# Kernel tuning notes

Measured on AMD Instinct MI355X. Metric: run time of the kernel, lower is better.

## Reference

```python
import jax, jax.numpy as jnp
import numpy as np

D_MODEL = 512
NUM_HEADS = 8
D_K = D_MODEL // NUM_HEADS  # 64
LN_EPS = 1e-5


def setup_inputs() -> dict:
    key = jax.random.key(0)
    ks = jax.random.split(key, 6)
    B, S, D = 8, 1024, D_MODEL
    scale = 1.0 / np.sqrt(D)
    return {
        "query": jax.random.normal(ks[0], (B, S, D), jnp.float32),
        "key": jax.random.normal(ks[1], (B, S, D), jnp.float32),
        "value": jax.random.normal(ks[2], (B, S, D), jnp.float32),
        "Wq": jax.random.normal(ks[3], (D, D), jnp.float32) * scale,
        "bq": jnp.zeros((D,), jnp.float32),
        "Wk": jax.random.normal(ks[4], (D, D), jnp.float32) * scale,
        "bk": jnp.zeros((D,), jnp.float32),
        "Wo": jax.random.normal(ks[5], (D, D * NUM_HEADS), jnp.float32) * (1.0 / np.sqrt(D * NUM_HEADS)),
        "bo": jnp.zeros((D,), jnp.float32),
        "gamma": jnp.ones((D,), jnp.float32),
        "beta": jnp.zeros((D,), jnp.float32),
    }


def reference(query, key, value, Wq, bq, Wk, bk, Wo, bo, gamma, beta):
    B, S, D = value.shape
    h, dk = NUM_HEADS, D_K
    # QK projections -> [B, h, S, dk]
    q = (query @ Wq.T + bq).reshape(B, S, h, dk).transpose(0, 2, 1, 3)
    k = (key @ Wk.T + bk).reshape(B, S, h, dk).transpose(0, 2, 1, 3)
    # scaled dot-product scores [B, h, Sq, Sk]
    scores = jnp.einsum("bhqd,bhkd->bhqk", q, k) / jnp.sqrt(jnp.asarray(dk, q.dtype))
    attn = jax.nn.softmax(scores, axis=-1)
    # value broadcast across heads: value is [B, Sk, D] -> per-head output [B, h, Sq, D]
    x = jnp.einsum("bhqk,bkd->bhqd", attn, value)
    # concat heads -> [B, Sq, h*D], output projection back to D
    x = x.transpose(0, 2, 1, 3).reshape(B, S, h * D)
    x = x @ Wo.T + bo
    # residual + LayerNorm (dropout = identity in eval)
    y = value + x
    mu = jnp.mean(y, axis=-1, keepdims=True)
    var = jnp.var(y, axis=-1, keepdims=True)
    out = (y - mu) * jax.lax.rsqrt(var + LN_EPS) * gamma + beta
    return out, attn
```

## Files before the change

### kernel.cpp

```cpp
#include <hip/hip_runtime.h>
#include <hip/hip_bf16.h>

#define B_ 8
#define S_ 1024
#define D_ 512
#define H_ 8
#define DK_ 64
#define HD_ 4096

typedef __attribute__((ext_vector_type(8))) short bf16x8;
typedef __attribute__((ext_vector_type(4))) float f32x4;

static __device__ __forceinline__ unsigned short f2bf(float f) {
    unsigned u = __float_as_uint(f);
    unsigned r = (u + 0x7fffu + ((u >> 16) & 1u)) >> 16;
    return (unsigned short)r;
}

static __device__ __forceinline__ void gload16(const unsigned short* g, unsigned short* l) {
    __builtin_amdgcn_global_load_lds(
        (const __attribute__((address_space(1))) void*)g,
        (__attribute__((address_space(3))) void*)l, 16, 0, 0);
}

static __device__ __forceinline__ int plidx(int ql, int k) {
    return ql * 1024 + ((((k >> 3) ^ (ql & 7))) << 3) + (k & 7);
}

__global__ __launch_bounds__(256) void cvt_kernel(
    const float* __restrict__ src, unsigned short* __restrict__ dst)
{
    const size_t i = ((size_t)blockIdx.x * 256 + threadIdx.x) * 4;
    float4 v = *(const float4*)&src[i];
    ushort4 u = { f2bf(v.x), f2bf(v.y), f2bf(v.z), f2bf(v.w) };
    *(ushort4*)&dst[i] = u;
}

__global__ __launch_bounds__(256) void cvt2_kernel(
    const float* __restrict__ s0, unsigned short* __restrict__ d0,
    const float* __restrict__ s1, unsigned short* __restrict__ d1, int nb0)
{
    const bool first = (int)blockIdx.x < nb0;
    const float* s = first ? s0 : s1;
    unsigned short* d = first ? d0 : d1;
    const int bid = first ? blockIdx.x : blockIdx.x - nb0;
    const size_t i = ((size_t)bid * 256 + threadIdx.x) * 4;
    float4 v = *(const float4*)&s[i];
    ushort4 u = { f2bf(v.x), f2bf(v.y), f2bf(v.z), f2bf(v.w) };
    *(ushort4*)&d[i] = u;
}

__global__ __launch_bounds__(256) void vt_kernel(
    const float* __restrict__ V, unsigned short* __restrict__ Vt)
{
    __shared__ float tile[32][33];
    const int b = blockIdx.z, s0 = blockIdx.x * 32, e0 = blockIdx.y * 32;
    const int t = threadIdx.x;
    const int r = t >> 3, c4 = (t & 7) * 4;
    float4 v = *(const float4*)&V[((size_t)b * S_ + s0 + r) * D_ + e0 + c4];
    tile[r][c4 + 0] = v.x; tile[r][c4 + 1] = v.y;
    tile[r][c4 + 2] = v.z; tile[r][c4 + 3] = v.w;
    __syncthreads();
    ushort4 u;
    u.x = f2bf(tile[c4 + 0][r]); u.y = f2bf(tile[c4 + 1][r]);
    u.z = f2bf(tile[c4 + 2][r]); u.w = f2bf(tile[c4 + 3][r]);
    *(ushort4*)&Vt[((size_t)b * D_ + e0 + r) * S_ + s0 + c4] = u;
}

template<int KDIM, int TN, int MODE>
__global__ __launch_bounds__(256) void gemm_t(
    const unsigned short* __restrict__ A, const unsigned short* __restrict__ Bw,
    const float* __restrict__ bias, const float* __restrict__ Vres,
    void* __restrict__ Out, float scale)
{
    constexpr int NB = 512 / TN;
    constexpr int CF = TN / 32;
    const int o = blockIdx.x;
    const int cpx = gridDim.x / 8;
    const int nb = (o % 8) * cpx + o / 8;
    const int m0 = (nb / NB) * 128;
    const int n0 = (nb % NB) * TN;

    __shared__ __align__(16) unsigned short As[2][128 * 32];
    __shared__ __align__(16) unsigned short Bs[2][TN * 32];

    const int t = threadIdx.x;
    const int wave = t >> 6, lane = t & 63;
    const int wr = wave >> 1, wc = wave & 1;
    const int lr = lane & 15, g = lane >> 4;
    const int gx = (g ^ (lr & 3)) << 3;

    f32x4 acc[4][CF];
    #pragma unroll
    for (int r = 0; r < 4; ++r)
        #pragma unroll
        for (int c = 0; c < CF; ++c) acc[r][c] = (f32x4){0.f, 0.f, 0.f, 0.f};

    const int sub = lane >> 2;
    const int cb  = (((lane & 3) ^ (sub & 3)) << 3);

    auto stage = [&](int buf, int k0) {
        #pragma unroll
        for (int s = 0; s < 2; ++s) {
            const int chunk = s * 4 + wave;
            const int row = chunk * 16 + sub;
            if constexpr (MODE == 0) {
                gload16(&A[(size_t)(m0 + row) * KDIM + k0 + cb], &As[buf][chunk * 512]);
            } else {
                const int m = m0 + row;
                const int bb = m >> 10, ss = m & 1023;
                const int h = k0 >> 9;
                gload16(&A[(((size_t)(bb * H_ + h)) * S_ + ss) * D_ + (k0 & 511) + cb],
                        &As[buf][chunk * 512]);
            }
        }
        #pragma unroll
        for (int s = 0; s < TN / 64; ++s) {
            const int chunk = s * 4 + wave;
            const int row = chunk * 16 + sub;
            gload16(&Bw[(size_t)(n0 + row) * KDIM + k0 + cb], &Bs[buf][chunk * 512]);
        }
    };
    auto compute = [&](int cur) {
        bf16x8 af[4], bfr[CF];
        #pragma unroll
        for (int r = 0; r < 4; ++r)
            af[r] = *(const bf16x8*)&As[cur][(wr * 64 + r * 16 + lr) * 32 + gx];
        #pragma unroll
        for (int c = 0; c < CF; ++c)
            bfr[c] = *(const bf16x8*)&Bs[cur][(wc * (TN / 2) + c * 16 + lr) * 32 + gx];
        __builtin_amdgcn_s_setprio(1);
        #pragma unroll
        for (int c = 0; c < CF; ++c)
            #pragma unroll
            for (int r = 0; r < 4; ++r)
                acc[r][c] = __builtin_amdgcn_mfma_f32_16x16x32_bf16(af[r], bfr[c], acc[r][c], 0, 0, 0);
        __builtin_amdgcn_s_setprio(0);
    };

    const int NT = KDIM / 32;
    stage(0, 0);
    __syncthreads();
    int cur = 0;
    for (int tt = 0; tt < NT - 1; ++tt) {
        stage(cur ^ 1, (tt + 1) * 32);
        compute(cur);
        __syncthreads();
        cur ^= 1;
    }
    compute(cur);

    float bn[CF];
    #pragma unroll
    for (int c = 0; c < CF; ++c) bn[c] = bias[n0 + wc * (TN / 2) + c * 16 + lr];

    #pragma unroll
    for (int r = 0; r < 4; ++r) {
        #pragma unroll
        for (int c = 0; c < CF; ++c) {
            const int n = n0 + wc * (TN / 2) + c * 16 + lr;
            #pragma unroll
            for (int i = 0; i < 4; ++i) {
                const int m = m0 + wr * 64 + r * 16 + g * 4 + i;
                if constexpr (MODE == 0) {
                    const int srow = m & 1023, bb = m >> 10;
                    const int h = n >> 6, dk = n & 63;
                    ((unsigned short*)Out)[(((size_t)(bb * H_ + h)) * S_ + srow) * DK_ + dk] =
                        f2bf((acc[r][c][i] + bn[c]) * scale);
                } else {
                    const size_t oo = (size_t)m * D_ + n;
                    ((float*)Out)[oo] = acc[r][c][i] + bn[c] + Vres[oo];
                }
            }
        }
    }
}

__global__ __launch_bounds__(1024, 4) void fused_attn(
    const unsigned short* __restrict__ Qbf,
    const unsigned short* __restrict__ Kbf,
    const unsigned short* __restrict__ Vt,
    float* __restrict__ attn,
    unsigned short* __restrict__ AV)
{
    const int o = blockIdx.x;
    const int nb = (o & 7) * 128 + (o >> 3);
    const int bh = nb >> 4;
    const int q0 = (nb & 15) * 64;
    const int b = bh >> 3;
    const unsigned short* Qb = Qbf + (size_t)bh * S_ * DK_;
    const unsigned short* Kb = Kbf + (size_t)bh * S_ * DK_;
    const unsigned short* Vb = Vt + (size_t)b * D_ * S_;
    float* outp = attn + ((size_t)bh << 20);

    __shared__ unsigned short PL[64 * 1024];
    __shared__ float redm[64][16];
    __shared__ float rowm[64];

    const int t = threadIdx.x;
    const int wave = t >> 6, lane = t & 63;
    const int wcol = wave * 64;
    const int lr = lane & 15;
    const int g  = lane >> 4;

    f32x4 acc[4][4];
    #pragma unroll
    for (int r = 0; r < 4; ++r)
        #pragma unroll
        for (int c = 0; c < 4; ++c) acc[r][c] = (f32x4){0.f, 0.f, 0.f, 0.f};

    #pragma unroll
    for (int kk = 0; kk < 2; ++kk) {
        bf16x8 af[4];
        #pragma unroll
        for (int r = 0; r < 4; ++r)
            af[r] = *(const bf16x8*)&Kb[(size_t)(wcol + r * 16 + lr) * DK_ + kk * 32 + g * 8];
        bf16x8 qf[4];
        #pragma unroll
        for (int c = 0; c < 4; ++c)
            qf[c] = *(const bf16x8*)&Qb[(size_t)(q0 + c * 16 + lr) * DK_ + kk * 32 + g * 8];
        __builtin_amdgcn_s_setprio(1);
        #pragma unroll
        for (int r = 0; r < 4; ++r)
            #pragma unroll
            for (int c = 0; c < 4; ++c)
                acc[r][c] = __builtin_amdgcn_mfma_f32_16x16x32_bf16(af[r], qf[c], acc[r][c], 0, 0, 0);
        __builtin_amdgcn_s_setprio(0);
    }

    float mloc[4];
    #pragma unroll
    for (int c = 0; c < 4; ++c) {
        float m = acc[0][c][0];
        #pragma unroll
        for (int r = 0; r < 4; ++r)
            #pragma unroll
            for (int i = 0; i < 4; ++i) m = fmaxf(m, acc[r][c][i]);
        m = fmaxf(m, __shfl_xor(m, 16));
        m = fmaxf(m, __shfl_xor(m, 32));
        mloc[c] = m;
    }
    if (lane < 16) {
        #pragma unroll
        for (int c = 0; c < 4; ++c) redm[c * 16 + lane][wave] = mloc[c];
    }
    __syncthreads();
    if (t < 64) {
        float m = redm[t][0];
        #pragma unroll
        for (int w = 1; w < 16; ++w) m = fmaxf(m, redm[t][w]);
        rowm[t] = m;
    }
    __syncthreads();
    float sloc[4];
    #pragma unroll
    for (int c = 0; c < 4; ++c) {
        const float m = rowm[c * 16 + lr];
        float s = 0.f;
        #pragma unroll
        for (int r = 0; r < 4; ++r)
            #pragma unroll
            for (int i = 0; i < 4; ++i) {
                float p = __expf(acc[r][c][i] - m);
                acc[r][c][i] = p;
                s += p;
            }
        s += __shfl_xor(s, 16);
        s += __shfl_xor(s, 32);
        sloc[c] = s;
    }
    __syncthreads();
    if (lane < 16) {
        #pragma unroll
        for (int c = 0; c < 4; ++c) redm[c * 16 + lane][wave] = sloc[c];
    }
    __syncthreads();
    if (t < 64) {
        float s = redm[t][0];
        #pragma unroll
        for (int w = 1; w < 16; ++w) s += redm[t][w];
        rowm[t] = 1.0f / s;
    }
    __syncthreads();

    #pragma unroll
    for (int c = 0; c < 4; ++c) {
        const int ql = c * 16 + lr;
        const float ri = rowm[ql];
        #pragma unroll
        for (int r = 0; r < 4; ++r) {
            f32x4 v = acc[r][c];
            v[0] *= ri; v[1] *= ri; v[2] *= ri; v[3] *= ri;
            const int k = wcol + r * 16 + g * 4;
            unsigned p01, p23;
            asm("v_cvt_pk_bf16_f32 %0, %1, %2" : "=v"(p01) : "v"(v[0]), "v"(v[1]));
            asm("v_cvt_pk_bf16_f32 %0, %1, %2" : "=v"(p23) : "v"(v[2]), "v"(v[3]));
            uint2 pk = { p01, p23 };
            *(uint2*)&PL[plidx(ql, k)] = pk;
        }
    }
    __syncthreads();

    #pragma unroll
    for (int jj = 0; jj < 4; ++jj) {
        const int row = wave * 4 + jj;
        const int ps = lane ^ (row & 7);
        float* rowp = outp + ((size_t)(q0 + row) << 10);
        uint4 u0 = *(const uint4*)&PL[row * 1024 + (ps << 3)];
        uint4 u1 = *(const uint4*)&PL[row * 1024 + ((64 + ps) << 3)];
        f32x4 f0, f1, f2, f3;
        f0[0] = __uint_as_float((u0.x & 0xffffu) << 16);
        f0[1] = __uint_as_float(u0.x & 0xffff0000u);
        f0[2] = __uint_as_float((u0.y & 0xffffu) << 16);
        f0[3] = __uint_as_float(u0.y & 0xffff0000u);
        f1[0] = __uint_as_float((u0.z & 0xffffu) << 16);
        f1[1] = __uint_as_float(u0.z & 0xffff0000u);
        f1[2] = __uint_as_float((u0.w & 0xffffu) << 16);
        f1[3] = __uint_as_float(u0.w & 0xffff0000u);
        f2[0] = __uint_as_float((u1.x & 0xffffu) << 16);
        f2[1] = __uint_as_float(u1.x & 0xffff0000u);
        f2[2] = __uint_as_float((u1.y & 0xffffu) << 16);
        f2[3] = __uint_as_float(u1.y & 0xffff0000u);
        f3[0] = __uint_as_float((u1.z & 0xffffu) << 16);
        f3[1] = __uint_as_float(u1.z & 0xffff0000u);
        f3[2] = __uint_as_float((u1.w & 0xffffu) << 16);
        f3[3] = __uint_as_float(u1.w & 0xffff0000u);
        const int k0f = lane * 8;
        __builtin_nontemporal_store(f0, (f32x4*)&rowp[k0f]);
        __builtin_nontemporal_store(f1, (f32x4*)&rowp[k0f + 4]);
        __builtin_nontemporal_store(f2, (f32x4*)&rowp[512 + k0f]);
        __builtin_nontemporal_store(f3, (f32x4*)&rowp[512 + k0f + 4]);
    }

    const int we = wave * 32;
    f32x4 accv[4][2];
    #pragma unroll
    for (int r = 0; r < 4; ++r)
        #pragma unroll
        for (int c = 0; c < 2; ++c) accv[r][c] = (f32x4){0.f, 0.f, 0.f, 0.f};

    const unsigned short* vp0 = Vb + (size_t)(we + lr) * S_ + g * 8;
    const unsigned short* vp1 = Vb + (size_t)(we + 16 + lr) * S_ + g * 8;
    bf16x8 vf0 = *(const bf16x8*)vp0;
    bf16x8 vf1 = *(const bf16x8*)vp1;

    for (int k0 = 0; k0 < S_; k0 += 32) {
        bf16x8 nv0, nv1;
        const int kn = k0 + 32;
        if (kn < S_) {
            nv0 = *(const bf16x8*)(vp0 + kn);
            nv1 = *(const bf16x8*)(vp1 + kn);
        }
        bf16x8 pa[4];
        #pragma unroll
        for (int r = 0; r < 4; ++r)
            pa[r] = *(const bf16x8*)&PL[plidx(r * 16 + lr, k0 + g * 8)];
        __builtin_amdgcn_s_setprio(1);
        #pragma unroll
        for (int r = 0; r < 4; ++r)
            accv[r][0] = __builtin_amdgcn_mfma_f32_16x16x32_bf16(pa[r], vf0, accv[r][0], 0, 0, 0);
        #pragma unroll
        for (int r = 0; r < 4; ++r)
            accv[r][1] = __builtin_amdgcn_mfma_f32_16x16x32_bf16(pa[r], vf1, accv[r][1], 0, 0, 0);
        __builtin_amdgcn_s_setprio(0);
        if (kn < S_) { vf0 = nv0; vf1 = nv1; }
    }

    __syncthreads();
    unsigned short* PL2 = PL;
    #pragma unroll
    for (int r = 0; r < 4; ++r)
        #pragma unroll
        for (int c = 0; c < 2; ++c) {
            const int e = we + c * 16 + lr;
            #pragma unroll
            for (int i = 0; i < 4; ++i) {
                const int row = r * 16 + g * 4 + i;
                PL2[row * 520 + e] = f2bf(accv[r][c][i]);
            }
        }
    __syncthreads();
    {
        const int row = t >> 4;
        unsigned short* avp = AV + ((size_t)bh * S_ + q0 + row) * D_;
        #pragma unroll
        for (int j = 0; j < 4; ++j) {
            const int e0 = (t & 15) * 8 + j * 128;
            uint4 u = *(const uint4*)&PL2[row * 520 + e0];
            *(uint4*)&avp[e0] = u;
        }
    }
}

__global__ __launch_bounds__(256) void ln_kernel(
    float* __restrict__ Y, const float* __restrict__ gamma,
    const float* __restrict__ beta)
{
    const int lane = threadIdx.x & 63;
    const int wave = threadIdx.x >> 6;
    const size_t row = (size_t)blockIdx.x * 4 + wave;
    float* p = Y + row * D_;
    float4 v0 = *(float4*)&p[lane * 4];
    float4 v1 = *(float4*)&p[256 + lane * 4];
    float s = v0.x + v0.y + v0.z + v0.w + v1.x + v1.y + v1.z + v1.w;
    float q = v0.x * v0.x + v0.y * v0.y + v0.z * v0.z + v0.w * v0.w +
              v1.x * v1.x + v1.y * v1.y + v1.z * v1.z + v1.w * v1.w;
    #pragma unroll
    for (int m = 1; m < 64; m <<= 1) {
        s += __shfl_xor(s, m);
        q += __shfl_xor(q, m);
    }
    const float mu  = s * (1.f / 512.f);
    const float var = q * (1.f / 512.f) - mu * mu;
    const float r = rsqrtf(var + 1e-5f);
    const float4 g0 = *(const float4*)&gamma[lane * 4];
    const float4 g1 = *(const float4*)&gamma[256 + lane * 4];
    const float4 b0 = *(const float4*)&beta[lane * 4];
    const float4 b1 = *(const float4*)&beta[256 + lane * 4];
    v0.x = (v0.x - mu) * r * g0.x + b0.x;
    v0.y = (v0.y - mu) * r * g0.y + b0.y;
    v0.z = (v0.z - mu) * r * g0.z + b0.z;
    v0.w = (v0.w - mu) * r * g0.w + b0.w;
    v1.x = (v1.x - mu) * r * g1.x + b1.x;
    v1.y = (v1.y - mu) * r * g1.y + b1.y;
    v1.z = (v1.z - mu) * r * g1.z + b1.z;
    v1.w = (v1.w - mu) * r * g1.w + b1.w;
    *(float4*)&p[lane * 4] = v0;
    *(float4*)&p[256 + lane * 4] = v1;
}

extern "C" void kernel_launch(void* const* d_in, const int* in_sizes, int n_in,
                              void* d_out, int out_size, void* d_ws, size_t ws_size,
                              hipStream_t stream)
{
    const float* query = (const float*)d_in[0];
    const float* key   = (const float*)d_in[1];
    const float* value = (const float*)d_in[2];
    const float* Wq    = (const float*)d_in[3];
    const float* bq    = (const float*)d_in[4];
    const float* Wk    = (const float*)d_in[5];
    const float* bk    = (const float*)d_in[6];
    const float* Wo    = (const float*)d_in[7];
    const float* bo    = (const float*)d_in[8];
    const float* gamma = (const float*)d_in[9];
    const float* beta  = (const float*)d_in[10];

    float* out  = (float*)d_out;
    float* attn = out + (size_t)B_ * S_ * D_;
    char*  attnB = (char*)attn;

    char* ws = (char*)d_ws;
    unsigned short* AV   = (unsigned short*)ws;
    unsigned short* Vt   = (unsigned short*)(ws + ((size_t)64 << 20));
    unsigned short* Wobf = (unsigned short*)(ws + ((size_t)72 << 20));
    unsigned short* Qbf  = (unsigned short*)d_out;
    unsigned short* Kbf  = (unsigned short*)d_out + ((size_t)4 << 20);
    unsigned short* Xq   = (unsigned short*)(attnB + ((size_t)200 << 20));
    unsigned short* Xk   = (unsigned short*)(attnB + ((size_t)210 << 20));
    unsigned short* Wqbf = (unsigned short*)(attnB + ((size_t)220 << 20));
    unsigned short* Wkbf = (unsigned short*)(attnB + ((size_t)221 << 20));

    cvt2_kernel<<<8192, 256, 0, stream>>>(query, Xq, key, Xk, 4096);
    cvt2_kernel<<<512,  256, 0, stream>>>(Wq, Wqbf, Wk, Wkbf, 256);
    cvt_kernel<<<2048, 256, 0, stream>>>(Wo, Wobf);
    vt_kernel<<<dim3(32, 16, 8), 256, 0, stream>>>(value, Vt);
    gemm_t<512, 64, 0><<<512, 256, 0, stream>>>(Xq, Wqbf, bq, nullptr, (void*)Qbf, 0.125f);
    gemm_t<512, 64, 0><<<512, 256, 0, stream>>>(Xk, Wkbf, bk, nullptr, (void*)Kbf, 1.0f);
    fused_attn<<<1024, 1024, 0, stream>>>(Qbf, Kbf, Vt, attn, AV);
    gemm_t<4096, 64, 1><<<512, 256, 0, stream>>>(AV, Wobf, bo, value, (void*)out, 0.f);
    ln_kernel<<<2048, 256, 0, stream>>>(out, gamma, beta);
}
```

Before: 366.3 us.

## Warp-specialize attention tail: half the waves store probabilities, half compute PV

The block's waves are split into two roles. Waves 8-15 convert and write the bf16 attention probabilities from LDS to the fp32 attention output, now with plain stores instead of nontemporal ones. Waves 0-7 compute the attn·V product over 64 output columns each, with no register prefetch of V, and write bf16 results straight to global memory without a second LDS staging pass and its barriers. The aim is to overlap the large attention-matrix write with the PV MFMA work. The cost is scattered 2-byte global stores, twice the accumulator registers per PV wave, and only half the waves feeding the MFMA units.

```diff
diff --git a/kernel.cpp b/kernel.cpp
--- a/kernel.cpp
+++ b/kernel.cpp
@@ -301,93 +301,72 @@
     }
     __syncthreads();
 
-    #pragma unroll
-    for (int jj = 0; jj < 4; ++jj) {
-        const int row = wave * 4 + jj;
-        const int ps = lane ^ (row & 7);
-        float* rowp = outp + ((size_t)(q0 + row) << 10);
-        uint4 u0 = *(const uint4*)&PL[row * 1024 + (ps << 3)];
-        uint4 u1 = *(const uint4*)&PL[row * 1024 + ((64 + ps) << 3)];
-        f32x4 f0, f1, f2, f3;
-        f0[0] = __uint_as_float((u0.x & 0xffffu) << 16);
-        f0[1] = __uint_as_float(u0.x & 0xffff0000u);
-        f0[2] = __uint_as_float((u0.y & 0xffffu) << 16);
-        f0[3] = __uint_as_float(u0.y & 0xffff0000u);
-        f1[0] = __uint_as_float((u0.z & 0xffffu) << 16);
-        f1[1] = __uint_as_float(u0.z & 0xffff0000u);
-        f1[2] = __uint_as_float((u0.w & 0xffffu) << 16);
-        f1[3] = __uint_as_float(u0.w & 0xffff0000u);
-        f2[0] = __uint_as_float((u1.x & 0xffffu) << 16);
-        f2[1] = __uint_as_float(u1.x & 0xffff0000u);
-        f2[2] = __uint_as_float((u1.y & 0xffffu) << 16);
-        f2[3] = __uint_as_float(u1.y & 0xffff0000u);
-        f3[0] = __uint_as_float((u1.z & 0xffffu) << 16);
-        f3[1] = __uint_as_float(u1.z & 0xffff0000u);
-        f3[2] = __uint_as_float((u1.w & 0xffffu) << 16);
-        f3[3] = __uint_as_float(u1.w & 0xffff0000u);
-        const int k0f = lane * 8;
-        __builtin_nontemporal_store(f0, (f32x4*)&rowp[k0f]);
-        __builtin_nontemporal_store(f1, (f32x4*)&rowp[k0f + 4]);
-        __builtin_nontemporal_store(f2, (f32x4*)&rowp[512 + k0f]);
-        __builtin_nontemporal_store(f3, (f32x4*)&rowp[512 + k0f + 4]);
-    }
-
-    const int we = wave * 32;
-    f32x4 accv[4][2];
-    #pragma unroll
-    for (int r = 0; r < 4; ++r)
-        #pragma unroll
-        for (int c = 0; c < 2; ++c) accv[r][c] = (f32x4){0.f, 0.f, 0.f, 0.f};
-
-    const unsigned short* vp0 = Vb + (size_t)(we + lr) * S_ + g * 8;
-    const unsigned short* vp1 = Vb + (size_t)(we + 16 + lr) * S_ + g * 8;
-    bf16x8 vf0 = *(const bf16x8*)vp0;
-    bf16x8 vf1 = *(const bf16x8*)vp1;
-
-    for (int k0 = 0; k0 < S_; k0 += 32) {
-        bf16x8 nv0, nv1;
-        const int kn = k0 + 32;
-        if (kn < S_) {
-            nv0 = *(const bf16x8*)(vp0 + kn);
-            nv1 = *(const bf16x8*)(vp1 + kn);
-        }
-        bf16x8 pa[4];
-        #pragma unroll
-        for (int r = 0; r < 4; ++r)
-            pa[r] = *(const bf16x8*)&PL[plidx(r * 16 + lr, k0 + g * 8)];
-        __builtin_amdgcn_s_setprio(1);
-        #pragma unroll
-        for (int r = 0; r < 4; ++r)
-            accv[r][0] = __builtin_amdgcn_mfma_f32_16x16x32_bf16(pa[r], vf0, accv[r][0], 0, 0, 0);
-        #pragma unroll
-        for (int r = 0; r < 4; ++r)
-            accv[r][1] = __builtin_amdgcn_mfma_f32_16x16x32_bf16(pa[r], vf1, accv[r][1], 0, 0, 0);
-        __builtin_amdgcn_s_setprio(0);
-        if (kn < S_) { vf0 = nv0; vf1 = nv1; }
-    }
-
-    __syncthreads();
-    unsigned short* PL2 = PL;
-    #pragma unroll
-    for (int r = 0; r < 4; ++r)
-        #pragma unroll
-        for (int c = 0; c < 2; ++c) {
-            const int e = we + c * 16 + lr;
-            #pragma unroll
-            for (int i = 0; i < 4; ++i) {
-                const int row = r * 16 + g * 4 + i;
-                PL2[row * 520 + e] = f2bf(accv[r][c][i]);
+    if (wave >= 8) {
+        #pragma unroll
+        for (int jj = 0; jj < 8; ++jj) {
+            const int row = (wave - 8) * 8 + jj;
+            const int ps = lane ^ (row & 7);
+            float* rowp = outp + ((size_t)(q0 + row) << 10);
+            uint4 u0 = *(const uint4*)&PL[row * 1024 + (ps << 3)];
+            uint4 u1 = *(const uint4*)&PL[row * 1024 + ((64 + ps) << 3)];
+            f32x4 f0, f1, f2, f3;
+            f0[0] = __uint_as_float((u0.x & 0xffffu) << 16);
+            f0[1] = __uint_as_float(u0.x & 0xffff0000u);
+            f0[2] = __uint_as_float((u0.y & 0xffffu) << 16);
+            f0[3] = __uint_as_float(u0.y & 0xffff0000u);
+            f1[0] = __uint_as_float((u0.z & 0xffffu) << 16);
+            f1[1] = __uint_as_float(u0.z & 0xffff0000u);
+            f1[2] = __uint_as_float((u0.w & 0xffffu) << 16);
+            f1[3] = __uint_as_float(u0.w & 0xffff0000u);
+            f2[0] = __uint_as_float((u1.x & 0xffffu) << 16);
+            f2[1] = __uint_as_float(u1.x & 0xffff0000u);
+            f2[2] = __uint_as_float((u1.y & 0xffffu) << 16);
+            f2[3] = __uint_as_float(u1.y & 0xffff0000u);
+            f3[0] = __uint_as_float((u1.z & 0xffffu) << 16);
+            f3[1] = __uint_as_float(u1.z & 0xffff0000u);
+            f3[2] = __uint_as_float((u1.w & 0xffffu) << 16);
+            f3[3] = __uint_as_float(u1.w & 0xffff0000u);
+            const int k0f = lane * 8;
+            *(f32x4*)&rowp[k0f]           = f0;
+            *(f32x4*)&rowp[k0f + 4]       = f1;
+            *(f32x4*)&rowp[512 + k0f]     = f2;
+            *(f32x4*)&rowp[512 + k0f + 4] = f3;
+        }
+    } else {
+        const int we = wave * 64;
+        f32x4 accv[4][4];
+        #pragma unroll
+        for (int r = 0; r < 4; ++r)
+            #pragma unroll
+            for (int c = 0; c < 4; ++c) accv[r][c] = (f32x4){0.f, 0.f, 0.f, 0.f};
+
+        for (int k0 = 0; k0 < S_; k0 += 32) {
+            bf16x8 pa[4];
+            #pragma unroll
+            for (int r = 0; r < 4; ++r)
+                pa[r] = *(const bf16x8*)&PL[plidx(r * 16 + lr, k0 + g * 8)];
+            __builtin_amdgcn_s_setprio(1);
+            #pragma unroll
+            for (int c = 0; c < 4; ++c) {
+                bf16x8 vf = *(const bf16x8*)&Vb[(size_t)(we + c * 16 + lr) * S_ + k0 + g * 8];
+                #pragma unroll
+                for (int r = 0; r < 4; ++r)
+                    accv[r][c] = __builtin_amdgcn_mfma_f32_16x16x32_bf16(pa[r], vf, accv[r][c], 0, 0, 0);
             }
-        }
-    __syncthreads();
-    {
-        const int row = t >> 4;
-        unsigned short* avp = AV + ((size_t)bh * S_ + q0 + row) * D_;
-        #pragma unroll
-        for (int j = 0; j < 4; ++j) {
-            const int e0 = (t & 15) * 8 + j * 128;
-            uint4 u = *(const uint4*)&PL2[row * 520 + e0];
-            *(uint4*)&avp[e0] = u;
+            __builtin_amdgcn_s_setprio(0);
+        }
+
+        #pragma unroll
+        for (int r = 0; r < 4; ++r) {
+            #pragma unroll
+            for (int c = 0; c < 4; ++c) {
+                const int e = we + c * 16 + lr;
+                #pragma unroll
+                for (int i = 0; i < 4; ++i) {
+                    const int row = q0 + r * 16 + g * 4 + i;
+                    AV[((size_t)bh * S_ + row) * D_ + e] = f2bf(accv[r][c][i]);
+                }
+            }
         }
     }
 }
```

Result: no change. 362.5 us (-1.0%).
